# Kernel tuning notes

Measured on AMD Instinct MI355X. Metric: run time of the kernel, lower is better.

Reference implementation:

```python
import jax, jax.numpy as jnp
import numpy as np

D_MODEL = 768
NUM_HEADS = 12
D_HEAD = D_MODEL // NUM_HEADS


def setup_inputs() -> dict:
    key = jax.random.key(0)
    ks = jax.random.split(key, 12)
    B, S = 2, 2048
    s = 1.0 / np.sqrt(D_MODEL)
    inp = {
        "query": jax.random.normal(ks[0], (B, S, D_MODEL), dtype=jnp.float32),
        "key": jax.random.normal(ks[1], (B, S, D_MODEL), dtype=jnp.float32),
        "value": jax.random.normal(ks[2], (B, S, D_MODEL), dtype=jnp.float32),
        "mask": jax.random.randint(ks[3], (B, 1, 1, S), 0, 2, dtype=jnp.int32),
        "Wq": jax.random.normal(ks[4], (D_MODEL, D_MODEL), dtype=jnp.float32) * s,
        "bq": jnp.zeros((D_MODEL,), dtype=jnp.float32),
        "Wk": jax.random.normal(ks[5], (D_MODEL, D_MODEL), dtype=jnp.float32) * s,
        "bk": jnp.zeros((D_MODEL,), dtype=jnp.float32),
        "Wv": jax.random.normal(ks[6], (D_MODEL, D_MODEL), dtype=jnp.float32) * s,
        "bv": jnp.zeros((D_MODEL,), dtype=jnp.float32),
        "Wo": jax.random.normal(ks[7], (D_MODEL, D_MODEL), dtype=jnp.float32) * s,
        "bo": jnp.zeros((D_MODEL,), dtype=jnp.float32),
    }
    return inp


def _split_heads(x):
    # [B, S, D] -> [B, H, S, Dh]
    B, S, _ = x.shape
    return x.reshape(B, S, NUM_HEADS, D_HEAD).transpose(0, 2, 1, 3)


def reference(query, key, value, mask, Wq, bq, Wk, bk, Wv, bv, Wo, bo):
    q = _split_heads(query @ Wq + bq)
    k = _split_heads(key @ Wk + bk)
    v = _split_heads(value @ Wv + bv)
    scores = jnp.einsum("bhqd,bhkd->bhqk", q, k) / jnp.sqrt(jnp.float32(D_HEAD))
    scores = jnp.where(mask == 0, -jnp.inf, scores)
    attn = jax.nn.softmax(scores, axis=-1)  # dropout is identity at inference
    ctx = jnp.einsum("bhqk,bhkd->bhqd", attn, v)
    B, _, S, _ = ctx.shape
    ctx = ctx.transpose(0, 2, 1, 3).reshape(B, S, D_MODEL)
    return ctx @ Wo + bo
```

## Files before the change

### kernel.cpp

```cpp
#include <hip/hip_runtime.h>
#include <stdint.h>

#define D_MODEL 768
#define SEQ     2048
#define BATCH   2
#define NHEAD   12
#define DHEAD   64
#define MROWS   (BATCH * SEQ)

typedef __bf16 bf16x8 __attribute__((ext_vector_type(8)));
typedef float  f32x4  __attribute__((ext_vector_type(4)));
typedef float  f32x16 __attribute__((ext_vector_type(16)));
typedef unsigned short u16;
typedef u16 u16x4 __attribute__((ext_vector_type(4)));
typedef uint32_t u32;

__device__ __forceinline__ u16 f32_to_bf16(float x) {
    u32 u = __float_as_uint(x);
    u32 r = (u + 0x7FFFu + ((u >> 16) & 1u)) >> 16;
    return (u16)r;
}
__device__ __forceinline__ float bf16_to_f32(u16 h) {
    return __uint_as_float(((u32)h) << 16);
}
__device__ __forceinline__ void split2(float x, u16 &hi, u16 &lo) {
    hi = f32_to_bf16(x);
    lo = f32_to_bf16(x - bf16_to_f32(hi));
}
__device__ __forceinline__ u32 pack2t(float a, float b) {
    return __builtin_amdgcn_perm(__float_as_uint(b), __float_as_uint(a), 0x07060302u);
}

__device__ __forceinline__ void stage16(const u16* g, const u16* l) {
    __builtin_amdgcn_global_load_lds(
        (const __attribute__((address_space(1))) u32*)g,
        (__attribute__((address_space(3))) u32*)l,
        16, 0, 0);
}

#define SRC_C8(lane)  ((((lane) & 3) ^ (((lane) >> 3) & 3)) * 8)
#define RD_C8(quad, l16) (((quad) ^ (((l16) >> 1) & 3)) * 8)

#define QSCALE 0.1803368801111204f
#define MSHIFT 20.0f

__global__ void prep_all(const float* __restrict__ q, const float* __restrict__ k,
                         const float* __restrict__ v, u16* __restrict__ xbase,
                         const float* __restrict__ Wq, const float* __restrict__ Wk,
                         const float* __restrict__ Wv, const float* __restrict__ Wo,
                         u16* __restrict__ wtbase,
                         const int* __restrict__ Mask, float* __restrict__ BiasM)
{
    __shared__ float tile[32][33];
    const int bx = blockIdx.x;
    if (bx < 9216) {
        const int t = bx / 3072;
        const float* src = (t == 0) ? q : (t == 1) ? k : v;
        const size_t P = (size_t)MROWS * D_MODEL;
        u16* xh = xbase + (size_t)t * 2 * P;
        u16* xl = xh + P;
        size_t idx = ((size_t)(bx % 3072) * 256 + threadIdx.x) * 4;
        float4 val = *reinterpret_cast<const float4*>(&src[idx]);
        float vv[4] = {val.x, val.y, val.z, val.w};
        u16x4 h4, l4;
        #pragma unroll
        for (int j = 0; j < 4; ++j) { u16 h, l; split2(vv[j], h, l); h4[j] = h; l4[j] = l; }
        *reinterpret_cast<u16x4*>(&xh[idx]) = h4;
        *reinterpret_cast<u16x4*>(&xl[idx]) = l4;
    } else if (bx < 11520) {
        int r = bx - 9216;
        int w = r / 576; r %= 576;
        int ky = r / 24, nx = r % 24;
        const float* W = (w == 0) ? Wq : (w == 1) ? Wk : (w == 2) ? Wv : Wo;
        const size_t WP = (size_t)D_MODEL * D_MODEL;
        u16* th = wtbase + (size_t)w * 2 * WP;
        u16* tl = th + WP;
        const int tx = threadIdx.x & 31, ty = threadIdx.x >> 5;
        const int n0 = nx * 32, k0 = ky * 32;
        #pragma unroll
        for (int rr = 0; rr < 4; ++rr) {
            int kk = k0 + ty + rr * 8;
            tile[ty + rr * 8][tx] = W[(size_t)kk * D_MODEL + n0 + tx];
        }
        __syncthreads();
        #pragma unroll
        for (int rr = 0; rr < 4; ++rr) {
            int n = n0 + ty + rr * 8;
            float val = tile[tx][ty + rr * 8];
            u16 h, l; split2(val, h, l);
            th[(size_t)n * D_MODEL + k0 + tx] = h;
            tl[(size_t)n * D_MODEL + k0 + tx] = l;
        }
    } else {
        int i = (bx - 11520) * 256 + threadIdx.x;
        BiasM[i] = (Mask[i] == 0) ? -3e38f : -MSHIFT;
    }
}

__global__ __launch_bounds__(256, 4) void gemm3(
    const u16* __restrict__ Ah0, const u16* __restrict__ Al0,
    const u16* __restrict__ Ah1, const u16* __restrict__ Al1,
    const u16* __restrict__ Ah2, const u16* __restrict__ Al2,
    const u16* __restrict__ Bh0, const u16* __restrict__ Bl0,
    const u16* __restrict__ Bh1, const u16* __restrict__ Bl1,
    const u16* __restrict__ Bh2, const u16* __restrict__ Bl2,
    const float* __restrict__ bias0, const float* __restrict__ bias1,
    const float* __restrict__ bias2,
    u16* __restrict__ Qhl, u16* __restrict__ Khl, u16* __restrict__ Vt,
    float* __restrict__ Out, int mode)
{
    const int z = (mode == 3) ? 3 : (int)blockIdx.z;
    const u16 *GAh, *GAl, *GBh, *GBl; const float* Bias;
    if (z == 1)      { GAh = Ah1; GAl = Al1; GBh = Bh1; GBl = Bl1; Bias = bias1; }
    else if (z == 2) { GAh = Ah2; GAl = Al2; GBh = Bh2; GBl = Bl2; Bias = bias2; }
    else             { GAh = Ah0; GAl = Al0; GBh = Bh0; GBl = Bl0; Bias = bias0; }

    const int m0 = blockIdx.x * 128;
    const int n0 = blockIdx.y * 64;
    const int tid  = threadIdx.x;
    const int wave = tid >> 6, lane = tid & 63;
    const int quad = lane >> 4, l16 = lane & 15;
    const int wm = wave & 1, wn = wave >> 1;

    __shared__ u16 sAh[128 * 32];
    __shared__ u16 sAl[128 * 32];
    __shared__ u16 sBh[64 * 32];
    __shared__ u16 sBl[64 * 32];

    const int srow = lane >> 2;
    const int sc8  = SRC_C8(lane);
    const int rc8  = RD_C8(quad, l16);

    f32x4 acc[4][2] = {};

    for (int k0 = 0; k0 < D_MODEL; k0 += 32) {
        {
            #pragma unroll
            for (int i = 0; i < 2; ++i) {
                int row = wave * 32 + i * 16 + srow;
                size_t ga = (size_t)(m0 + row) * D_MODEL + k0 + sc8;
                int ldst = (wave * 32 + i * 16) * 32;
                stage16(&GAh[ga], &sAh[ldst]);
                stage16(&GAl[ga], &sAl[ldst]);
            }
            int row = wave * 16 + srow;
            size_t gb = (size_t)(n0 + row) * D_MODEL + k0 + sc8;
            int ldst = (wave * 16) * 32;
            stage16(&GBh[gb], &sBh[ldst]);
            stage16(&GBl[gb], &sBl[ldst]);
        }
        asm volatile("s_waitcnt vmcnt(0)" ::: "memory");
        __syncthreads();

        bf16x8 afh[4], afl[4], bfh[2], bfl[2];
        #pragma unroll
        for (int t = 0; t < 4; ++t) {
            int ar = wm * 64 + t * 16 + l16;
            afh[t] = *reinterpret_cast<const bf16x8*>(&sAh[ar * 32 + rc8]);
            afl[t] = *reinterpret_cast<const bf16x8*>(&sAl[ar * 32 + rc8]);
        }
        #pragma unroll
        for (int t = 0; t < 2; ++t) {
            int bc = wn * 32 + t * 16 + l16;
            bfh[t] = *reinterpret_cast<const bf16x8*>(&sBh[bc * 32 + rc8]);
            bfl[t] = *reinterpret_cast<const bf16x8*>(&sBl[bc * 32 + rc8]);
        }
        #pragma unroll
        for (int mt = 0; mt < 4; ++mt) {
            #pragma unroll
            for (int nt = 0; nt < 2; ++nt) {
                f32x4 a = acc[mt][nt];
                a = __builtin_amdgcn_mfma_f32_16x16x32_bf16(afh[mt], bfh[nt], a, 0, 0, 0);
                a = __builtin_amdgcn_mfma_f32_16x16x32_bf16(afh[mt], bfl[nt], a, 0, 0, 0);
                a = __builtin_amdgcn_mfma_f32_16x16x32_bf16(afl[mt], bfh[nt], a, 0, 0, 0);
                acc[mt][nt] = a;
            }
        }
        __syncthreads();
    }

    #pragma unroll
    for (int nt = 0; nt < 2; ++nt) {
        int n = n0 + wn * 32 + nt * 16 + l16;
        float bv = Bias[n];
        #pragma unroll
        for (int mt = 0; mt < 4; ++mt) {
            #pragma unroll
            for (int r = 0; r < 4; ++r) {
                int m = m0 + wm * 64 + mt * 16 + quad * 4 + r;
                float v = acc[mt][nt][r] + bv;
                if (mode == 3) {
                    Out[(size_t)m * D_MODEL + n] = v;
                } else {
                    int b = m >> 11, s = m & (SEQ - 1);
                    int h = n >> 6, d = n & 63;
                    size_t bh = (size_t)(b * NHEAD + h);
                    if (z == 0) {
                        u16 hi, lo; split2(v * QSCALE, hi, lo);
                        u16* base = &Qhl[(bh * SEQ + s) * 128];
                        base[d] = hi; base[d + 64] = lo;
                    } else if (z == 1) {
                        u16 hi, lo; split2(v, hi, lo);
                        u16* base = &Khl[(bh * SEQ + s) * 128];
                        base[d] = hi; base[d + 64] = lo;
                    } else {
                        Vt[(bh * DHEAD + d) * SEQ + s] = f32_to_bf16(v);
                    }
                }
            }
        }
    }
}

__global__ __launch_bounds__(256, 4) void gemm_out64(
    const u16* __restrict__ GAh, const u16* __restrict__ GAl,
    const u16* __restrict__ GBh, const u16* __restrict__ GBl,
    const float* __restrict__ Bias, float* __restrict__ Out)
{
    const int m0 = blockIdx.x * 64;
    const int n0 = blockIdx.y * 64;
    const int tid  = threadIdx.x;
    const int wave = tid >> 6, lane = tid & 63;
    const int quad = lane >> 4, l16 = lane & 15;
    const int wm = wave & 1, wn = wave >> 1;

    __shared__ u16 sAh[64 * 32];
    __shared__ u16 sAl[64 * 32];
    __shared__ u16 sBh[64 * 32];
    __shared__ u16 sBl[64 * 32];

    const int srow = lane >> 2;
    const int sc8  = SRC_C8(lane);
    const int rc8  = RD_C8(quad, l16);

    f32x4 acc[2][2] = {};

    for (int k0 = 0; k0 < D_MODEL; k0 += 32) {
        {
            int row = wave * 16 + srow;
            size_t ga = (size_t)(m0 + row) * D_MODEL + k0 + sc8;
            size_t gb = (size_t)(n0 + row) * D_MODEL + k0 + sc8;
            int ldst = (wave * 16) * 32;
            stage16(&GAh[ga], &sAh[ldst]);
            stage16(&GAl[ga], &sAl[ldst]);
            stage16(&GBh[gb], &sBh[ldst]);
            stage16(&GBl[gb], &sBl[ldst]);
        }
        asm volatile("s_waitcnt vmcnt(0)" ::: "memory");
        __syncthreads();

        bf16x8 afh[2], afl[2], bfh[2], bfl[2];
        #pragma unroll
        for (int t = 0; t < 2; ++t) {
            int ar = wm * 32 + t * 16 + l16;
            afh[t] = *reinterpret_cast<const bf16x8*>(&sAh[ar * 32 + rc8]);
            afl[t] = *reinterpret_cast<const bf16x8*>(&sAl[ar * 32 + rc8]);
        }
        #pragma unroll
        for (int t = 0; t < 2; ++t) {
            int bc = wn * 32 + t * 16 + l16;
            bfh[t] = *reinterpret_cast<const bf16x8*>(&sBh[bc * 32 + rc8]);
            bfl[t] = *reinterpret_cast<const bf16x8*>(&sBl[bc * 32 + rc8]);
        }
        #pragma unroll
        for (int mt = 0; mt < 2; ++mt) {
            #pragma unroll
            for (int nt = 0; nt < 2; ++nt) {
                f32x4 a = acc[mt][nt];
                a = __builtin_amdgcn_mfma_f32_16x16x32_bf16(afh[mt], bfh[nt], a, 0, 0, 0);
                a = __builtin_amdgcn_mfma_f32_16x16x32_bf16(afh[mt], bfl[nt], a, 0, 0, 0);
                a = __builtin_amdgcn_mfma_f32_16x16x32_bf16(afl[mt], bfh[nt], a, 0, 0, 0);
                acc[mt][nt] = a;
            }
        }
        __syncthreads();
    }

    #pragma unroll
    for (int nt = 0; nt < 2; ++nt) {
        int n = n0 + wn * 32 + nt * 16 + l16;
        float bv = Bias[n];
        #pragma unroll
        for (int mt = 0; mt < 2; ++mt) {
            #pragma unroll
            for (int r = 0; r < 4; ++r) {
                int m = m0 + wm * 32 + mt * 16 + quad * 4 + r;
                Out[(size_t)m * D_MODEL + n] = acc[mt][nt][r] + bv;
            }
        }
    }
}

__global__ __launch_bounds__(256, 3) void attn_kernel(
    const u16* __restrict__ Qhl, const u16* __restrict__ Khl, const u16* __restrict__ Vt,
    const float* __restrict__ BiasM, float* __restrict__ Opart,
    float* __restrict__ Lpart)
{
    const int flat = blockIdx.x;
    const int wk   = (flat & 7) * 96 + (flat >> 3);
    const int qt   = wk & 15;
    const int grp  = wk >> 4;
    const int bh   = grp % 24;
    const int half = grp / 24;
    const int b    = bh / NHEAD;
    const int tid  = threadIdx.x;
    const int wave = tid >> 6, lane = tid & 63;
    const int l32  = lane & 31;
    const int hi5  = lane >> 5;
    const int xorv = (l32 >> 1) & 3;

    __shared__ u16 sK[2][4 * 2048];
    __shared__ u16 sV[2][2 * 2048];

    const u16* qbase = &Qhl[((size_t)bh * SEQ + qt * 128 + wave * 32 + l32) * 128];
    bf16x8 qh[4], ql[4];
    #pragma unroll
    for (int ds = 0; ds < 4; ++ds) {
        qh[ds] = *reinterpret_cast<const bf16x8*>(&qbase[ds * 16 + hi5 * 8]);
        ql[ds] = *reinterpret_cast<const bf16x8*>(&qbase[64 + ds * 16 + hi5 * 8]);
    }

    union OU { u16 u[8]; bf16x8 v; } onesu;
    #pragma unroll
    for (int j = 0; j < 8; ++j) onesu.u[j] = 0x3F80;
    const bf16x8 ones = onesu.v;

    f32x16 oacc[2] = {};
    f32x16 lacc = {};

    const float* biasb = &BiasM[b * SEQ];
    const int strow = wave * 16 + (lane >> 2);
    const int stc8  = SRC_C8(lane);
    const u16* kgb = &Khl[(size_t)bh * SEQ * 128];
    const u16* vgb = &Vt[(size_t)bh * DHEAD * SEQ];

    const int kvbeg = half * (SEQ / 2);

    #pragma unroll
    for (int j = 0; j < 4; ++j)
        stage16(&kgb[(size_t)(kvbeg + strow) * 128 + j * 32 + stc8],
                &sK[0][j * 2048 + wave * 512]);
    #pragma unroll
    for (int j = 0; j < 2; ++j)
        stage16(&vgb[(size_t)strow * SEQ + kvbeg + j * 32 + stc8],
                &sV[0][j * 2048 + wave * 512]);

    for (int it = 0; it < 16; ++it) {
        const int kv0 = kvbeg + it * 64;
        asm volatile("s_waitcnt vmcnt(0)" ::: "memory");
        __syncthreads();

        if (it + 1 < 16) {
            const int kvn = kv0 + 64;
            u16* dK = sK[(it + 1) & 1];
            u16* dV = sV[(it + 1) & 1];
            #pragma unroll
            for (int j = 0; j < 4; ++j)
                stage16(&kgb[(size_t)(kvn + strow) * 128 + j * 32 + stc8],
                        &dK[j * 2048 + wave * 512]);
            #pragma unroll
            for (int j = 0; j < 2; ++j)
                stage16(&vgb[(size_t)strow * SEQ + kvn + j * 32 + stc8],
                        &dV[j * 2048 + wave * 512]);
        }
        const u16* cK = sK[it & 1];
        const u16* cV = sV[it & 1];

        u32 pk[2][8];
        #pragma unroll
        for (int t = 0; t < 2; ++t) {
            f32x16 s;
            #pragma unroll
            for (int g = 0; g < 4; ++g) {
                float4 b4 = *reinterpret_cast<const float4*>(
                    &biasb[kv0 + t * 32 + 8 * g + 4 * hi5]);
                s[4 * g + 0] = b4.x; s[4 * g + 1] = b4.y;
                s[4 * g + 2] = b4.z; s[4 * g + 3] = b4.w;
            }
            const int rowb = (t * 32 + l32) * 32;
            __builtin_amdgcn_s_setprio(1);
            #pragma unroll
            for (int ds = 0; ds < 4; ++ds) {
                const int c8  = ((((ds & 1) * 2 + hi5) ^ xorv) * 8);
                const int off = (ds >> 1) * 2048 + rowb + c8;
                bf16x8 kh = *reinterpret_cast<const bf16x8*>(&cK[off]);
                bf16x8 kl = *reinterpret_cast<const bf16x8*>(&cK[4096 + off]);
                s = __builtin_amdgcn_mfma_f32_32x32x16_bf16(kh, qh[ds], s, 0, 0, 0);
                s = __builtin_amdgcn_mfma_f32_32x32x16_bf16(kh, ql[ds], s, 0, 0, 0);
                s = __builtin_amdgcn_mfma_f32_32x32x16_bf16(kl, qh[ds], s, 0, 0, 0);
            }
            __builtin_amdgcn_s_setprio(0);
            #pragma unroll
            for (int m = 0; m < 8; ++m)
                pk[t][m] = pack2t(exp2f(s[2 * m]), exp2f(s[2 * m + 1]));
        }

        union FU { u32 u[4]; bf16x8 v; } fr[4];
        #pragma unroll
        for (int t = 0; t < 2; ++t) {
            u32 a0 = pk[t][0], b0 = pk[t][2];
            u32 a1 = pk[t][1], b1 = pk[t][3];
            u32 a2 = pk[t][4], b2 = pk[t][6];
            u32 a3 = pk[t][5], b3 = pk[t][7];
            asm volatile("v_permlane32_swap_b32 %0, %1" : "+v"(a0), "+v"(b0));
            asm volatile("v_permlane32_swap_b32 %0, %1" : "+v"(a1), "+v"(b1));
            asm volatile("v_permlane32_swap_b32 %0, %1" : "+v"(a2), "+v"(b2));
            asm volatile("v_permlane32_swap_b32 %0, %1" : "+v"(a3), "+v"(b3));
            fr[2 * t].u[0] = a0; fr[2 * t].u[1] = a1;
            fr[2 * t].u[2] = b0; fr[2 * t].u[3] = b1;
            fr[2 * t + 1].u[0] = a2; fr[2 * t + 1].u[1] = a3;
            fr[2 * t + 1].u[2] = b2; fr[2 * t + 1].u[3] = b3;
        }

        __builtin_amdgcn_s_setprio(1);
        #pragma unroll
        for (int dt = 0; dt < 2; ++dt) {
            const int drow = (dt * 32 + l32) * 32;
            #pragma unroll
            for (int sl = 0; sl < 4; ++sl) {
                const int c8  = ((((sl & 1) * 2 + hi5) ^ xorv) * 8);
                const int off = (sl >> 1) * 2048 + drow + c8;
                bf16x8 vb = *reinterpret_cast<const bf16x8*>(&cV[off]);
                oacc[dt] = __builtin_amdgcn_mfma_f32_32x32x16_bf16(vb, fr[sl].v, oacc[dt], 0, 0, 0);
            }
        }
        #pragma unroll
        for (int sl = 0; sl < 4; ++sl)
            lacc = __builtin_amdgcn_mfma_f32_32x32x16_bf16(ones, fr[sl].v, lacc, 0, 0, 0);
        __builtin_amdgcn_s_setprio(0);
    }

    {
        size_t rowb = ((size_t)(half * (BATCH * NHEAD) + bh)) * SEQ
                    + qt * 128 + wave * 32 + l32;
        float* ob = &Opart[rowb * 64];
        #pragma unroll
        for (int dt = 0; dt < 2; ++dt) {
            #pragma unroll
            for (int g = 0; g < 4; ++g) {
                f32x4 o4 = { oacc[dt][4 * g + 0], oacc[dt][4 * g + 1],
                             oacc[dt][4 * g + 2], oacc[dt][4 * g + 3] };
                *reinterpret_cast<f32x4*>(&ob[dt * 32 + 8 * g + 4 * hi5]) = o4;
            }
        }
        if (lane < 32) Lpart[rowb] = lacc[0];
    }
}

__global__ void attn_combine(const float* __restrict__ Opart,
                             const float* __restrict__ Lpart,
                             u16* __restrict__ CTXh, u16* __restrict__ CTXl)
{
    const int NROW = BATCH * NHEAD * SEQ;
    int t = blockIdx.x * 256 + threadIdx.x;
    int row = t >> 4;
    int d0 = (t & 15) << 2;
    float inv = 1.f / (Lpart[row] + Lpart[NROW + row]);
    f32x4 O0 = *reinterpret_cast<const f32x4*>(&Opart[(size_t)row * 64 + d0]);
    f32x4 O1 = *reinterpret_cast<const f32x4*>(&Opart[((size_t)NROW + row) * 64 + d0]);
    int bh = row >> 11, q = row & (SEQ - 1);
    int b = bh / NHEAD, h = bh % NHEAD;
    size_t off = ((size_t)(b * SEQ + q)) * D_MODEL + h * DHEAD + d0;
    u16x4 h4, l4;
    #pragma unroll
    for (int j = 0; j < 4; ++j) {
        float val = (O0[j] + O1[j]) * inv;
        u16 hi, lo; split2(val, hi, lo);
        h4[j] = hi; l4[j] = lo;
    }
    *reinterpret_cast<u16x4*>(&CTXh[off]) = h4;
    *reinterpret_cast<u16x4*>(&CTXl[off]) = l4;
}

extern "C" void kernel_launch(void* const* d_in, const int* in_sizes, int n_in,
                              void* d_out, int out_size, void* d_ws, size_t ws_size,
                              hipStream_t stream)
{
    const float* query = (const float*)d_in[0];
    const float* key   = (const float*)d_in[1];
    const float* value = (const float*)d_in[2];
    const int*   mask  = (const int*)d_in[3];
    const float* Wq = (const float*)d_in[4];
    const float* bq = (const float*)d_in[5];
    const float* Wk = (const float*)d_in[6];
    const float* bk = (const float*)d_in[7];
    const float* Wv = (const float*)d_in[8];
    const float* bv = (const float*)d_in[9];
    const float* Wo = (const float*)d_in[10];
    const float* bo = (const float*)d_in[11];

    char* ws = (char*)d_ws;
    const size_t P2  = (size_t)MROWS * D_MODEL * 2;
    const size_t WP2 = (size_t)D_MODEL * D_MODEL * 2;

    u16* Xbase = (u16*)ws;
    u16* Xh_q = Xbase;                       u16* Xl_q = (u16*)((char*)Xh_q + P2);
    u16* Xh_k = (u16*)((char*)Xbase + 2*P2); u16* Xl_k = (u16*)((char*)Xh_k + P2);
    u16* Xh_v = (u16*)((char*)Xbase + 4*P2); u16* Xl_v = (u16*)((char*)Xh_v + P2);

    char* wtb = ws + 6 * P2;
    u16* Wh_q = (u16*)wtb;                   u16* Wl_q = (u16*)(wtb + WP2);
    u16* Wh_k = (u16*)(wtb + 2*WP2);         u16* Wl_k = (u16*)(wtb + 3*WP2);
    u16* Wh_v = (u16*)(wtb + 4*WP2);         u16* Wl_v = (u16*)(wtb + 5*WP2);
    u16* Wh_o = (u16*)(wtb + 6*WP2);         u16* Wl_o = (u16*)(wtb + 7*WP2);

    char* qb = wtb + 8 * WP2;
    const size_t QK_BYTES = (size_t)BATCH * NHEAD * SEQ * 128 * 2;
    u16* QhlBuf = (u16*)qb;
    u16* KhlBuf = (u16*)(qb + QK_BYTES);
    u16* VtBuf  = (u16*)(qb + 2 * QK_BYTES);

    char* tail = qb + 2 * QK_BYTES + QK_BYTES / 2;
    float* BiasM = (float*)tail;
    float* Lpart = (float*)(tail + 16384);

    float* Opart = (float*)Xh_k;
    u16* CTXh = Xh_q; u16* CTXl = Xl_q;

    float* out = (float*)d_out;
    dim3 blk(256, 1, 1);

    prep_all<<<dim3(11536), blk, 0, stream>>>(
        query, key, value, Xbase, Wq, Wk, Wv, Wo, (u16*)wtb, mask, BiasM);

    gemm3<<<dim3(32, 12, 3), blk, 0, stream>>>(
        Xh_q, Xl_q, Xh_k, Xl_k, Xh_v, Xl_v,
        Wh_q, Wl_q, Wh_k, Wl_k, Wh_v, Wl_v,
        bq, bk, bv, QhlBuf, KhlBuf, VtBuf, nullptr, 0);

    attn_kernel<<<dim3(768), blk, 0, stream>>>(
        QhlBuf, KhlBuf, VtBuf, BiasM, Opart, Lpart);

    attn_combine<<<dim3(3072), blk, 0, stream>>>(Opart, Lpart, CTXh, CTXl);

    gemm_out64<<<dim3(64, 12), blk, 0, stream>>>(
        CTXh, CTXl, Wh_o, Wl_o, bo, out);
}
```

Baseline: 264.9 us.

## Retile QKV projection GEMM to 64x192 tiles with XCD-aware block remapping

```diff
diff --git a/kernel.cpp b/kernel.cpp
--- a/kernel.cpp
+++ b/kernel.cpp
@@ -97,7 +97,7 @@
     }
 }
 
-__global__ __launch_bounds__(256, 4) void gemm3(
+__global__ __launch_bounds__(256, 2) void gemm3(
     const u16* __restrict__ Ah0, const u16* __restrict__ Al0,
     const u16* __restrict__ Ah1, const u16* __restrict__ Al1,
     const u16* __restrict__ Ah2, const u16* __restrict__ Al2,
@@ -106,69 +106,74 @@
     const u16* __restrict__ Bh2, const u16* __restrict__ Bl2,
     const float* __restrict__ bias0, const float* __restrict__ bias1,
     const float* __restrict__ bias2,
-    u16* __restrict__ Qhl, u16* __restrict__ Khl, u16* __restrict__ Vt,
-    float* __restrict__ Out, int mode)
+    u16* __restrict__ Qhl, u16* __restrict__ Khl, u16* __restrict__ Vt)
 {
-    const int z = (mode == 3) ? 3 : (int)blockIdx.z;
+    const int p  = blockIdx.x;
+    const int wk = (p & 7) * 96 + (p >> 3);
+    const int z  = wk / 256;
+    const int r  = wk % 256;
+    const int mx = r >> 2;
+    const int ny = r & 3;
+
     const u16 *GAh, *GAl, *GBh, *GBl; const float* Bias;
     if (z == 1)      { GAh = Ah1; GAl = Al1; GBh = Bh1; GBl = Bl1; Bias = bias1; }
     else if (z == 2) { GAh = Ah2; GAl = Al2; GBh = Bh2; GBl = Bl2; Bias = bias2; }
     else             { GAh = Ah0; GAl = Al0; GBh = Bh0; GBl = Bl0; Bias = bias0; }
 
-    const int m0 = blockIdx.x * 128;
-    const int n0 = blockIdx.y * 64;
+    const int m0 = mx * 64;
+    const int n0 = ny * 192;
     const int tid  = threadIdx.x;
     const int wave = tid >> 6, lane = tid & 63;
     const int quad = lane >> 4, l16 = lane & 15;
     const int wm = wave & 1, wn = wave >> 1;
 
-    __shared__ u16 sAh[128 * 32];
-    __shared__ u16 sAl[128 * 32];
-    __shared__ u16 sBh[64 * 32];
-    __shared__ u16 sBl[64 * 32];
+    __shared__ u16 sAh[64 * 32];
+    __shared__ u16 sAl[64 * 32];
+    __shared__ u16 sBh[192 * 32];
+    __shared__ u16 sBl[192 * 32];
 
     const int srow = lane >> 2;
     const int sc8  = SRC_C8(lane);
     const int rc8  = RD_C8(quad, l16);
 
-    f32x4 acc[4][2] = {};
+    f32x4 acc[2][6] = {};
 
     for (int k0 = 0; k0 < D_MODEL; k0 += 32) {
         {
-            #pragma unroll
-            for (int i = 0; i < 2; ++i) {
-                int row = wave * 32 + i * 16 + srow;
-                size_t ga = (size_t)(m0 + row) * D_MODEL + k0 + sc8;
-                int ldst = (wave * 32 + i * 16) * 32;
-                stage16(&GAh[ga], &sAh[ldst]);
-                stage16(&GAl[ga], &sAl[ldst]);
-            }
             int row = wave * 16 + srow;
-            size_t gb = (size_t)(n0 + row) * D_MODEL + k0 + sc8;
+            size_t ga = (size_t)(m0 + row) * D_MODEL + k0 + sc8;
             int ldst = (wave * 16) * 32;
-            stage16(&GBh[gb], &sBh[ldst]);
-            stage16(&GBl[gb], &sBl[ldst]);
+            stage16(&GAh[ga], &sAh[ldst]);
+            stage16(&GAl[ga], &sAl[ldst]);
+            #pragma unroll
+            for (int j = 0; j < 3; ++j) {
+                int brow = j * 64 + wave * 16 + srow;
+                size_t gb = (size_t)(n0 + brow) * D_MODEL + k0 + sc8;
+                int bdst = (j * 64 + wave * 16) * 32;
+                stage16(&GBh[gb], &sBh[bdst]);
+                stage16(&GBl[gb], &sBl[bdst]);
+            }
         }
         asm volatile("s_waitcnt vmcnt(0)" ::: "memory");
         __syncthreads();
 
-        bf16x8 afh[4], afl[4], bfh[2], bfl[2];
-        #pragma unroll
-        for (int t = 0; t < 4; ++t) {
-            int ar = wm * 64 + t * 16 + l16;
+        bf16x8 afh[2], afl[2], bfh[6], bfl[6];
+        #pragma unroll
+        for (int t = 0; t < 2; ++t) {
+            int ar = wm * 32 + t * 16 + l16;
             afh[t] = *reinterpret_cast<const bf16x8*>(&sAh[ar * 32 + rc8]);
             afl[t] = *reinterpret_cast<const bf16x8*>(&sAl[ar * 32 + rc8]);
         }
         #pragma unroll
-        for (int t = 0; t < 2; ++t) {
-            int bc = wn * 32 + t * 16 + l16;
+        for (int t = 0; t < 6; ++t) {
+            int bc = wn * 96 + t * 16 + l16;
             bfh[t] = *reinterpret_cast<const bf16x8*>(&sBh[bc * 32 + rc8]);
             bfl[t] = *reinterpret_cast<const bf16x8*>(&sBl[bc * 32 + rc8]);
         }
         #pragma unroll
-        for (int mt = 0; mt < 4; ++mt) {
-            #pragma unroll
-            for (int nt = 0; nt < 2; ++nt) {
+        for (int mt = 0; mt < 2; ++mt) {
+            #pragma unroll
+            for (int nt = 0; nt < 6; ++nt) {
                 f32x4 a = acc[mt][nt];
                 a = __builtin_amdgcn_mfma_f32_16x16x32_bf16(afh[mt], bfh[nt], a, 0, 0, 0);
                 a = __builtin_amdgcn_mfma_f32_16x16x32_bf16(afh[mt], bfl[nt], a, 0, 0, 0);
@@ -180,32 +185,28 @@
     }
 
     #pragma unroll
-    for (int nt = 0; nt < 2; ++nt) {
-        int n = n0 + wn * 32 + nt * 16 + l16;
+    for (int nt = 0; nt < 6; ++nt) {
+        int n = n0 + wn * 96 + nt * 16 + l16;
         float bv = Bias[n];
         #pragma unroll
-        for (int mt = 0; mt < 4; ++mt) {
-            #pragma unroll
-            for (int r = 0; r < 4; ++r) {
-                int m = m0 + wm * 64 + mt * 16 + quad * 4 + r;
-                float v = acc[mt][nt][r] + bv;
-                if (mode == 3) {
-                    Out[(size_t)m * D_MODEL + n] = v;
+        for (int mt = 0; mt < 2; ++mt) {
+            #pragma unroll
+            for (int rr = 0; rr < 4; ++rr) {
+                int m = m0 + wm * 32 + mt * 16 + quad * 4 + rr;
+                float v = acc[mt][nt][rr] + bv;
+                int b = m >> 11, s = m & (SEQ - 1);
+                int h = n >> 6, d = n & 63;
+                size_t bh = (size_t)(b * NHEAD + h);
+                if (z == 0) {
+                    u16 hi, lo; split2(v * QSCALE, hi, lo);
+                    u16* base = &Qhl[(bh * SEQ + s) * 128];
+                    base[d] = hi; base[d + 64] = lo;
+                } else if (z == 1) {
+                    u16 hi, lo; split2(v, hi, lo);
+                    u16* base = &Khl[(bh * SEQ + s) * 128];
+                    base[d] = hi; base[d + 64] = lo;
                 } else {
-                    int b = m >> 11, s = m & (SEQ - 1);
-                    int h = n >> 6, d = n & 63;
-                    size_t bh = (size_t)(b * NHEAD + h);
-                    if (z == 0) {
-                        u16 hi, lo; split2(v * QSCALE, hi, lo);
-                        u16* base = &Qhl[(bh * SEQ + s) * 128];
-                        base[d] = hi; base[d + 64] = lo;
-                    } else if (z == 1) {
-                        u16 hi, lo; split2(v, hi, lo);
-                        u16* base = &Khl[(bh * SEQ + s) * 128];
-                        base[d] = hi; base[d + 64] = lo;
-                    } else {
-                        Vt[(bh * DHEAD + d) * SEQ + s] = f32_to_bf16(v);
-                    }
+                    Vt[(bh * DHEAD + d) * SEQ + s] = f32_to_bf16(v);
                 }
             }
         }
@@ -523,10 +524,10 @@
     prep_all<<<dim3(11536), blk, 0, stream>>>(
         query, key, value, Xbase, Wq, Wk, Wv, Wo, (u16*)wtb, mask, BiasM);
 
-    gemm3<<<dim3(32, 12, 3), blk, 0, stream>>>(
+    gemm3<<<dim3(768), blk, 0, stream>>>(
         Xh_q, Xl_q, Xh_k, Xl_k, Xh_v, Xl_v,
         Wh_q, Wl_q, Wh_k, Wl_k, Wh_v, Wl_v,
-        bq, bk, bv, QhlBuf, KhlBuf, VtBuf, nullptr, 0);
+        bq, bk, bv, QhlBuf, KhlBuf, VtBuf);
 
     attn_kernel<<<dim3(768), blk, 0, stream>>>(
         QhlBuf, KhlBuf, VtBuf, BiasM, Opart, Lpart);
```

Result: no change. 261.6 us (median of 2 runs) (-1.2%).
